# Kernel optimization log

Hardware: AMD Instinct MI355X
Metric: run time of the kernel (lower is better)

Reference implementation:

```python
import jax, jax.numpy as jnp
import numpy as np

B, T, N_EMBED, HEADSIZE = 16, 2048, 1024, 128


def setup_inputs() -> dict:
    key = jax.random.key(0)
    kx, kq, kk, kv = jax.random.split(key, 4)
    x = jax.random.normal(kx, (B, T, N_EMBED), dtype=jnp.float32)
    # nn.Linear(n_embed, headsize, bias=False): y = x @ W, W stored [n_embed, headsize]
    s = (1.0 / np.sqrt(N_EMBED)).astype(np.float32)
    Wq = jax.random.normal(kq, (N_EMBED, HEADSIZE), dtype=jnp.float32) * s
    Wk = jax.random.normal(kk, (N_EMBED, HEADSIZE), dtype=jnp.float32) * s
    Wv = jax.random.normal(kv, (N_EMBED, HEADSIZE), dtype=jnp.float32) * s
    return {"x": x, "Wq": Wq, "Wk": Wk, "Wv": Wv}


def reference(x, Wq, Wk, Wv):
    Bsz, Tlen, C = x.shape
    q = x @ Wq  # [B, T, H]
    k = x @ Wk  # [B, T, H]
    v = x @ Wv  # [B, T, H]
    scale = C ** (-0.5)  # NOTE: original scales by n_embed**-0.5, not headsize**-0.5
    wt = jnp.einsum('bqh,bkh->bqk', q, k) * scale  # [B, T, T]
    causal = jnp.tril(jnp.ones((Tlen, Tlen), dtype=bool))
    wt = jnp.where(causal, wt, -jnp.inf)
    wt = jax.nn.softmax(wt, axis=-1)
    # dropout is identity in eval mode
    out = jnp.einsum('bqk,bkh->bqh', wt, v)  # [B, T, H]
    return out
```

## Files before the change

kernel.cpp:

```cpp
#include <hip/hip_runtime.h>
#include <hip/hip_bf16.h>

#define BATCH 16
#define TLEN 2048
#define CDIM 1024
#define HDIM 128

typedef __attribute__((ext_vector_type(8))) short bf16x8;
typedef __attribute__((ext_vector_type(4))) float f32x4;
typedef __attribute__((ext_vector_type(16))) float f32x16;
typedef __attribute__((ext_vector_type(4))) unsigned short u16x4;
typedef __attribute__((ext_vector_type(8))) unsigned short u16x8;

static __device__ __forceinline__ unsigned short f2bf(float f) {
    __hip_bfloat16 h = __float2bfloat16(f);
    return *(unsigned short*)&h;
}
static __device__ __forceinline__ unsigned pkbf(float a, float b) {
    return (unsigned)f2bf(a) | ((unsigned)f2bf(b) << 16);
}
static __device__ __forceinline__ int part_offs(int qc) {
    const int g = qc >> 2;
    return qc + 2 * g * (g - 1) + (qc & 3) * g;
}

typedef const __attribute__((address_space(1))) unsigned int* gas_t;
typedef __attribute__((address_space(3))) unsigned int* las_t;
static __device__ __forceinline__ void gl_lds16(const void* g, void* l) {
    __builtin_amdgcn_global_load_lds((gas_t)g, (las_t)l, 16, 0, 0);
}

static __device__ __forceinline__ void hard_barrier() {
    __builtin_amdgcn_sched_barrier(0);
    __builtin_amdgcn_s_barrier();
    __builtin_amdgcn_sched_barrier(0);
}

__global__ __launch_bounds__(256) void pack_w(
    const float* __restrict__ Wq, const float* __restrict__ Wk,
    const float* __restrict__ Wv, unsigned short* __restrict__ wtb)
{
    const int which = blockIdx.y;
    const float* W = (which == 0) ? Wq : (which == 1) ? Wk : Wv;
    const int n = blockIdx.x >> 2;
    const int k = (blockIdx.x & 3) * 256 + threadIdx.x;
    wtb[((size_t)which * 128 + n) * 1024 + k] = f2bf(W[(size_t)k * 128 + n]);
}

__global__ __launch_bounds__(512, 4) void qkv_fused(
    const float* __restrict__ x, const unsigned short* __restrict__ wtb,
    unsigned short* __restrict__ qb, unsigned short* __restrict__ kb,
    unsigned short* __restrict__ vtb)
{
    __shared__ __align__(16) unsigned short Ab[2][128 * 64];
    __shared__ __align__(16) unsigned short Bb[2][192 * 64];

    const int xcd = blockIdx.x & 7, s = blockIdx.x >> 3;
    const int m0 = (xcd * 32 + (s >> 1)) * 128;
    const int nh = s & 1;

    const int tid  = threadIdx.x;
    const int lane = tid & 63, wid = tid >> 6;
    const int wm = wid >> 2, wn = wid & 3;
    const int c = lane & 15, g = lane >> 4;

    const int arow = tid >> 2, aq = tid & 3;
    const float* xsrc = x + (size_t)(m0 + arow) * CDIM + aq * 16;

    f32x4 acc[4][3];
#pragma unroll
    for (int i = 0; i < 4; ++i)
#pragma unroll
        for (int j = 0; j < 3; ++j) acc[i][j] = (f32x4){0.f, 0.f, 0.f, 0.f};

    float4 As0, As1, As2, As3;

#define AISSUE(k0_)                                                          \
    { const float* s_ = xsrc + (k0_);                                        \
      As0 = *(const float4*)(s_);      As1 = *(const float4*)(s_ + 4);       \
      As2 = *(const float4*)(s_ + 8);  As3 = *(const float4*)(s_ + 12); }

#define AWRITE(bi_)                                                          \
    { u16x8 t0_, t1_;                                                        \
      t0_[0]=f2bf(As0.x); t0_[1]=f2bf(As0.y); t0_[2]=f2bf(As0.z); t0_[3]=f2bf(As0.w); \
      t0_[4]=f2bf(As1.x); t0_[5]=f2bf(As1.y); t0_[6]=f2bf(As1.z); t0_[7]=f2bf(As1.w); \
      t1_[0]=f2bf(As2.x); t1_[1]=f2bf(As2.y); t1_[2]=f2bf(As2.z); t1_[3]=f2bf(As2.w); \
      t1_[4]=f2bf(As3.x); t1_[5]=f2bf(As3.y); t1_[6]=f2bf(As3.z); t1_[7]=f2bf(As3.w); \
      char* ba_ = (char*)Ab[bi_] + arow * 128;                               \
      *(u16x8*)(ba_ + ((aq * 32 +  0) ^ ((arow & 7) << 4))) = t0_;           \
      *(u16x8*)(ba_ + ((aq * 32 + 16) ^ ((arow & 7) << 4))) = t1_; }

#define BISSUE(k0_, bi_)                                                     \
    { _Pragma("unroll")                                                      \
      for (int i_ = 0; i_ < 3; ++i_) {                                       \
          const int seg_ = wid * 3 + i_;                                     \
          const int row_ = seg_ * 8 + (lane >> 3);                           \
          const int gr_  = (lane & 7) ^ (row_ & 7);                          \
          gl_lds16(wtb + (size_t)(nh * 192 + row_) * 1024 + (k0_) + gr_ * 8, \
                   (char*)Bb[bi_] + seg_ * 1024);                            \
      } }

    AISSUE(0);
    BISSUE(0, 0);
    asm volatile("s_waitcnt vmcnt(3)" ::: "memory");
    AWRITE(0);
    asm volatile("s_waitcnt vmcnt(0) lgkmcnt(0)" ::: "memory");
    hard_barrier();

#pragma unroll 1
    for (int kt = 0; kt < 16; ++kt) {
        const int cur = kt & 1;
        if (kt < 15) {
            AISSUE((kt + 1) * 64);
            BISSUE((kt + 1) * 64, cur ^ 1);
        }

#pragma unroll
        for (int ks = 0; ks < 2; ++ks) {
            bf16x8 af[4], bf[3];
#pragma unroll
            for (int mf = 0; mf < 4; ++mf) {
                const int rm = wm * 64 + mf * 16 + c;
                af[mf] = *(const bf16x8*)((char*)Ab[cur] + rm * 128 +
                                          ((ks * 64 + g * 16) ^ ((rm & 7) << 4)));
            }
#pragma unroll
            for (int nf = 0; nf < 3; ++nf) {
                const int rn = wn * 48 + nf * 16 + c;
                bf[nf] = *(const bf16x8*)((char*)Bb[cur] + rn * 128 +
                                          ((ks * 64 + g * 16) ^ ((rn & 7) << 4)));
            }
            __builtin_amdgcn_s_setprio(1);
#pragma unroll
            for (int mf = 0; mf < 4; ++mf)
#pragma unroll
                for (int nf = 0; nf < 3; ++nf)
                    acc[mf][nf] = __builtin_amdgcn_mfma_f32_16x16x32_bf16(
                        af[mf], bf[nf], acc[mf][nf], 0, 0, 0);
            __builtin_amdgcn_s_setprio(0);
        }

        if (kt < 15) {
            asm volatile("s_waitcnt vmcnt(3)" ::: "memory");
            AWRITE(cur ^ 1);
            asm volatile("s_waitcnt vmcnt(0) lgkmcnt(0)" ::: "memory");
            hard_barrier();
        }
    }

#pragma unroll
    for (int mf = 0; mf < 4; ++mf) {
#pragma unroll
        for (int nf = 0; nf < 3; ++nf) {
            const int col0 = nh * 192 + wn * 48 + nf * 16;
            const int nt = col0 >> 7;
            const int nc = (col0 & 127) + c;
            const int m = m0 + wm * 64 + mf * 16 + g * 4;
            if (nt == 0) {
#pragma unroll
                for (int r = 0; r < 4; ++r)
                    qb[(size_t)(m + r) * HDIM + nc] = f2bf(acc[mf][nf][r] * 0.03125f);
            } else if (nt == 1) {
#pragma unroll
                for (int r = 0; r < 4; ++r)
                    kb[(size_t)(m + r) * HDIM + nc] = f2bf(acc[mf][nf][r]);
            } else {
                const int b = m >> 11, tl = m & (TLEN - 1);
                u16x4 o;
                o[0] = f2bf(acc[mf][nf][0]); o[1] = f2bf(acc[mf][nf][1]);
                o[2] = f2bf(acc[mf][nf][2]); o[3] = f2bf(acc[mf][nf][3]);
                *(u16x4*)(vtb + ((size_t)b * HDIM + nc) * TLEN + tl) = o;
            }
        }
    }
#undef AISSUE
#undef AWRITE
#undef BISSUE
}

__global__ __launch_bounds__(256, 2) void attn_partial(
    const short* __restrict__ qb, const short* __restrict__ kb,
    const short* __restrict__ vtb,
    unsigned short* __restrict__ Opart, float* __restrict__ mpart,
    float* __restrict__ lpart)
{
    const int kc = blockIdx.x;
    const int qc = blockIdx.y;
    const int b  = blockIdx.z;
    if (kc > (qc >> 2)) return;
    const int kv_base = kc * 512;
    const int qrel = qc * 128 - kv_base;
    int NT = (qrel >> 6) + 2; if (NT > 8) NT = 8;

    __shared__ unsigned short Ks[2][64 * 128];
    __shared__ unsigned short Vs[2][128 * 64];

    const int tid  = threadIdx.x;
    const int wid  = tid >> 6;
    const int lane = tid & 63;
    const int c5 = lane & 31, hi = lane >> 5;
    const int q0w = qc * 128 + wid * 32;
    const int qg  = q0w + c5;
    const int pidx = b * 40 + part_offs(qc) + kc;

    const short* Kb  = kb  + (size_t)b * TLEN * HDIM;
    const short* Vtb = vtb + (size_t)b * HDIM * TLEN;

    bf16x8 qf[8];
#pragma unroll
    for (int ks = 0; ks < 8; ++ks)
        qf[ks] = *(const bf16x8*)(qb + ((size_t)b * TLEN + qg) * HDIM + ks * 16 + hi * 8);

    bf16x8 kst[4], vst[4];

#define GLOAD(kv0_)                                                          \
    {                                                                        \
        _Pragma("unroll")                                                    \
        for (int it = 0; it < 4; ++it) {                                     \
            const int o = tid * 16 + it * 4096;                              \
            const int kr = o >> 8, kcb = o & 0xF0;                           \
            kst[it] = *(const bf16x8*)((const char*)Kb +                     \
                        (size_t)((kv0_) + kr) * 256 + kcb);                  \
            const int vr = o >> 7, vcb = o & 0x70;                           \
            vst[it] = *(const bf16x8*)((const char*)Vtb +                    \
                        (size_t)vr * (TLEN * 2) + (size_t)(kv0_) * 2 + vcb); \
        }                                                                    \
    }
#define SSTORE(bi_)                                                          \
    {                                                                        \
        _Pragma("unroll")                                                    \
        for (int it = 0; it < 4; ++it) {                                     \
            const int o = tid * 16 + it * 4096;                              \
            const int kr = o >> 8, kcb = o & 0xF0;                           \
            *(bf16x8*)((char*)Ks[bi_] + kr * 256 + (kcb ^ ((kr & 7) << 4))) = kst[it]; \
            const int vr = o >> 7, vcb = o & 0x70;                           \
            *(bf16x8*)((char*)Vs[bi_] + vr * 128 + (vcb ^ ((vr & 7) << 4))) = vst[it]; \
        }                                                                    \
    }

    GLOAD(kv_base);
    SSTORE(0);
    __syncthreads();

    f32x16 oacc[4];
#pragma unroll
    for (int i = 0; i < 4; ++i)
#pragma unroll
        for (int r = 0; r < 16; ++r) oacc[i][r] = 0.f;
    float m_r = -1e30f;
    float l_r = 0.f;

#pragma unroll 1
    for (int t = 0; t < NT; ++t) {
        const int bi = t & 1;
        if (t + 1 < NT) GLOAD(kv_base + 64 * (t + 1));

        const int kv0 = kv_base + 64 * t;
        if (kv0 <= q0w + 31) {
            f32x16 s0, s1;
#pragma unroll
            for (int r = 0; r < 16; ++r) { s0[r] = 0.f; s1[r] = 0.f; }
            __builtin_amdgcn_s_setprio(1);
#pragma unroll
            for (int ks = 0; ks < 8; ++ks) {
                const int col = ks * 32 + hi * 16;
                const int off0 = c5 * 256 + (col ^ ((c5 & 7) << 4));
                const int off1 = (32 + c5) * 256 + (col ^ ((c5 & 7) << 4));
                bf16x8 a0 = *(const bf16x8*)((char*)Ks[bi] + off0);
                bf16x8 a1 = *(const bf16x8*)((char*)Ks[bi] + off1);
                s0 = __builtin_amdgcn_mfma_f32_32x32x16_bf16(a0, qf[ks], s0, 0, 0, 0);
                s1 = __builtin_amdgcn_mfma_f32_32x32x16_bf16(a1, qf[ks], s1, 0, 0, 0);
            }
            __builtin_amdgcn_s_setprio(0);

            if (kv0 + 63 > q0w) {
#pragma unroll
                for (int r = 0; r < 16; ++r) {
                    const int key0 = kv0 + (r & 3) + 8 * (r >> 2) + 4 * hi;
                    if (key0 > qg)      s0[r] = -INFINITY;
                    if (key0 + 32 > qg) s1[r] = -INFINITY;
                }
            }

            float t8[8];
#pragma unroll
            for (int i = 0; i < 8; ++i)
                t8[i] = fmaxf(fmaxf(s0[2*i], s0[2*i+1]), fmaxf(s1[2*i], s1[2*i+1]));
            float smax = fmaxf(fmaxf(fmaxf(t8[0], t8[1]), fmaxf(t8[2], t8[3])),
                               fmaxf(fmaxf(t8[4], t8[5]), fmaxf(t8[6], t8[7])));
            smax = fmaxf(smax, __shfl_xor(smax, 32));

            const bool defer = __all(smax - m_r <= 8.0f);
            const float mnew = defer ? m_r : fmaxf(m_r, smax);
            if (!defer) {
                const float alpha = __expf(m_r - mnew);
                l_r *= alpha;
#pragma unroll
                for (int hb = 0; hb < 4; ++hb) oacc[hb] = oacc[hb] * alpha;
            }
            m_r = mnew;

#pragma unroll
            for (int r = 0; r < 16; ++r) {
                s0[r] = __expf(s0[r] - mnew);
                s1[r] = __expf(s1[r] - mnew);
            }
            float a8[8];
#pragma unroll
            for (int i = 0; i < 8; ++i)
                a8[i] = (s0[2*i] + s0[2*i+1]) + (s1[2*i] + s1[2*i+1]);
            float psum = ((a8[0] + a8[1]) + (a8[2] + a8[3])) +
                         ((a8[4] + a8[5]) + (a8[6] + a8[7]));
            psum += __shfl_xor(psum, 32);
            l_r += psum;

            bf16x8 pa[4];
#pragma unroll
            for (int kb2 = 0; kb2 < 2; ++kb2) {
#pragma unroll
                for (int par = 0; par < 2; ++par) {
                    const int e = par * 8;
                    float v0, v1, v2, v3, v4, v5, v6, v7;
                    if (kb2 == 0) {
                        v0=s0[e+0]; v1=s0[e+1]; v2=s0[e+2]; v3=s0[e+3];
                        v4=s0[e+4]; v5=s0[e+5]; v6=s0[e+6]; v7=s0[e+7];
                    } else {
                        v0=s1[e+0]; v1=s1[e+1]; v2=s1[e+2]; v3=s1[e+3];
                        v4=s1[e+4]; v5=s1[e+5]; v6=s1[e+6]; v7=s1[e+7];
                    }
                    const unsigned w0 = pkbf(v0, v1), w1 = pkbf(v2, v3);
                    const unsigned w2 = pkbf(v4, v5), w3 = pkbf(v6, v7);
                    const unsigned X0 = hi ? w0 : w2;
                    const unsigned X1 = hi ? w1 : w3;
                    const unsigned R0 = (unsigned)__shfl_xor((int)X0, 32);
                    const unsigned R1 = (unsigned)__shfl_xor((int)X1, 32);
                    union { unsigned w[4]; bf16x8 v; } uu;
                    uu.w[0] = hi ? R0 : w0;  uu.w[1] = hi ? R1 : w1;
                    uu.w[2] = hi ? w2 : R0;  uu.w[3] = hi ? w3 : R1;
                    pa[kb2 * 2 + par] = uu.v;
                }
            }

            __builtin_amdgcn_s_setprio(1);
#pragma unroll
            for (int hb = 0; hb < 4; ++hb) {
                const int row = hb * 32 + c5;
#pragma unroll
                for (int ks = 0; ks < 4; ++ks) {
                    const int off = row * 128 + ((ks * 32 + hi * 16) ^ ((row & 7) << 4));
                    bf16x8 va = *(const bf16x8*)((char*)Vs[bi] + off);
                    oacc[hb] = __builtin_amdgcn_mfma_f32_32x32x16_bf16(va, pa[ks], oacc[hb], 0, 0, 0);
                }
            }
            __builtin_amdgcn_s_setprio(0);
        }

        if (t + 1 < NT) {
            SSTORE(bi ^ 1);
            __syncthreads();
        }
    }

    __syncthreads();
    char* sl = (char*)Ks + wid * 8192;
#pragma unroll
    for (int hb = 0; hb < 4; ++hb)
#pragma unroll
        for (int rq = 0; rq < 4; ++rq) {
            u16x4 o4;
            o4[0] = f2bf(oacc[hb][rq * 4 + 0]);
            o4[1] = f2bf(oacc[hb][rq * 4 + 1]);
            o4[2] = f2bf(oacc[hb][rq * 4 + 2]);
            o4[3] = f2bf(oacc[hb][rq * 4 + 3]);
            const int off = c5 * 256 + ((hb * 64 + rq * 16 + hi * 8) ^ ((c5 & 7) << 4));
            *(u16x4*)(sl + off) = o4;
        }
    asm volatile("s_waitcnt lgkmcnt(0)" ::: "memory");
    __builtin_amdgcn_sched_barrier(0);

    const int qr = lane >> 1, hf = lane & 1;
    unsigned short* Og = Opart + (size_t)pidx * 128 * 128 +
                         (size_t)(wid * 32 + qr) * 128 + hf * 64;
#pragma unroll
    for (int i = 0; i < 8; ++i) {
        const int off = qr * 256 + ((hf * 128 + i * 16) ^ ((qr & 7) << 4));
        *(u16x8*)(Og + i * 8) = *(const u16x8*)(sl + off);
    }
    if (hi == 0) {
        mpart[(size_t)pidx * 128 + wid * 32 + c5] = m_r;
        lpart[(size_t)pidx * 128 + wid * 32 + c5] = l_r;
    }
#undef GLOAD
#undef SSTORE
}

__global__ __launch_bounds__(256) void attn_combine(
    const unsigned short* __restrict__ Opart, const float* __restrict__ mpart,
    const float* __restrict__ lpart, float* __restrict__ out)
{
    const int qc = blockIdx.x;
    const int b  = blockIdx.y;
    const int n  = (qc >> 2) + 1;
    const int base = b * 40 + part_offs(qc);
    const int t   = threadIdx.x;
    const int row = t >> 1;
    const int d0  = (t & 1) * 64;

    float mv[4], lv[4];
#pragma unroll
    for (int p = 0; p < 4; ++p) {
        mv[p] = (p < n) ? mpart[(size_t)(base + p) * 128 + row] : -INFINITY;
        lv[p] = (p < n) ? lpart[(size_t)(base + p) * 128 + row] : 0.f;
    }
    float M = fmaxf(fmaxf(mv[0], mv[1]), fmaxf(mv[2], mv[3]));
    float L = 0.f;
    float wv[4];
#pragma unroll
    for (int p = 0; p < 4; ++p) {
        wv[p] = (p < n) ? __expf(mv[p] - M) : 0.f;
        L += wv[p] * lv[p];
    }

    float acc[64];
#pragma unroll
    for (int i = 0; i < 64; ++i) acc[i] = 0.f;

    for (int p = 0; p < n; ++p) {
        const float w = wv[p];
        const bf16x8* src = (const bf16x8*)(Opart +
            ((size_t)(base + p) * 128 + row) * 128 + d0);
#pragma unroll
        for (int j = 0; j < 8; ++j) {
            bf16x8 v = src[j];
#pragma unroll
            for (int e = 0; e < 8; ++e) {
                union { unsigned u; float f; } xx;
                xx.u = ((unsigned)(unsigned short)v[e]) << 16;
                acc[j * 8 + e] += w * xx.f;
            }
        }
    }

    const float invL = 1.f / L;
    float4* dst = (float4*)(out + ((size_t)(b * TLEN + qc * 128 + row)) * 128 + d0);
#pragma unroll
    for (int i = 0; i < 16; ++i)
        dst[i] = make_float4(acc[4*i] * invL, acc[4*i+1] * invL,
                             acc[4*i+2] * invL, acc[4*i+3] * invL);
}

extern "C" void kernel_launch(void* const* d_in, const int* in_sizes, int n_in,
                              void* d_out, int out_size, void* d_ws, size_t ws_size,
                              hipStream_t stream)
{
    const float* x  = (const float*)d_in[0];
    const float* Wq = (const float*)d_in[1];
    const float* Wk = (const float*)d_in[2];
    const float* Wv = (const float*)d_in[3];
    float* outp = (float*)d_out;

    const size_t per = (size_t)BATCH * TLEN * HDIM;
    unsigned short* qb  = (unsigned short*)d_ws;
    unsigned short* kb  = qb + per;
    unsigned short* vtb = kb + per;
    unsigned short* wtb = vtb + per;
    unsigned short* Opart = wtb + 384 * 1024;
    float* mpart = (float*)(Opart + (size_t)640 * 128 * 128);
    float* lpart = mpart + (size_t)640 * 128;

    dim3 gw(512, 3);
    pack_w<<<gw, 256, 0, stream>>>(Wq, Wk, Wv, wtb);

    qkv_fused<<<512, 512, 0, stream>>>(x, wtb, qb, kb, vtb);

    dim3 g2(4, 16, BATCH);
    attn_partial<<<g2, 256, 0, stream>>>((const short*)qb, (const short*)kb,
                                         (const short*)vtb, Opart, mpart, lpart);

    dim3 g3(16, BATCH);
    attn_combine<<<g3, 256, 0, stream>>>(Opart, mpart, lpart, outp);
}
```

Baseline: 112.8 us.

## Double QKV projection M-tile to 256 rows to improve weight reuse

```diff
diff --git a/kernel.cpp b/kernel.cpp
--- a/kernel.cpp
+++ b/kernel.cpp
@@ -47,16 +47,16 @@
     wtb[((size_t)which * 128 + n) * 1024 + k] = f2bf(W[(size_t)k * 128 + n]);
 }
 
-__global__ __launch_bounds__(512, 4) void qkv_fused(
+__global__ __launch_bounds__(512, 2) void qkv_fused(
     const float* __restrict__ x, const unsigned short* __restrict__ wtb,
     unsigned short* __restrict__ qb, unsigned short* __restrict__ kb,
     unsigned short* __restrict__ vtb)
 {
-    __shared__ __align__(16) unsigned short Ab[2][128 * 64];
+    __shared__ __align__(16) unsigned short Ab[2][256 * 64];
     __shared__ __align__(16) unsigned short Bb[2][192 * 64];
 
     const int xcd = blockIdx.x & 7, s = blockIdx.x >> 3;
-    const int m0 = (xcd * 32 + (s >> 1)) * 128;
+    const int m0 = (xcd * 16 + (s >> 1)) * 256;
     const int nh = s & 1;
 
     const int tid  = threadIdx.x;
@@ -64,31 +64,37 @@
     const int wm = wid >> 2, wn = wid & 3;
     const int c = lane & 15, g = lane >> 4;
 
-    const int arow = tid >> 2, aq = tid & 3;
-    const float* xsrc = x + (size_t)(m0 + arow) * CDIM + aq * 16;
-
-    f32x4 acc[4][3];
-#pragma unroll
-    for (int i = 0; i < 4; ++i)
+    const int arow = tid >> 1, ah = tid & 1;
+    const float* xsrc = x + (size_t)(m0 + arow) * CDIM + ah * 32;
+
+    f32x4 acc[8][3];
+#pragma unroll
+    for (int i = 0; i < 8; ++i)
 #pragma unroll
         for (int j = 0; j < 3; ++j) acc[i][j] = (f32x4){0.f, 0.f, 0.f, 0.f};
 
-    float4 As0, As1, As2, As3;
+    float4 As0, As1, As2, As3, As4, As5, As6, As7;
 
 #define AISSUE(k0_)                                                          \
     { const float* s_ = xsrc + (k0_);                                        \
-      As0 = *(const float4*)(s_);      As1 = *(const float4*)(s_ + 4);       \
-      As2 = *(const float4*)(s_ + 8);  As3 = *(const float4*)(s_ + 12); }
+      As0 = *(const float4*)(s_);       As1 = *(const float4*)(s_ + 4);      \
+      As2 = *(const float4*)(s_ + 8);   As3 = *(const float4*)(s_ + 12);     \
+      As4 = *(const float4*)(s_ + 16);  As5 = *(const float4*)(s_ + 20);     \
+      As6 = *(const float4*)(s_ + 24);  As7 = *(const float4*)(s_ + 28); }
+
+#define CVT2(lo_, hi_, dst_)                                                 \
+    { u16x8 t_;                                                              \
+      t_[0]=f2bf(lo_.x); t_[1]=f2bf(lo_.y); t_[2]=f2bf(lo_.z); t_[3]=f2bf(lo_.w); \
+      t_[4]=f2bf(hi_.x); t_[5]=f2bf(hi_.y); t_[6]=f2bf(hi_.z); t_[7]=f2bf(hi_.w); \
+      *(u16x8*)(dst_) = t_; }
 
 #define AWRITE(bi_)                                                          \
-    { u16x8 t0_, t1_;                                                        \
-      t0_[0]=f2bf(As0.x); t0_[1]=f2bf(As0.y); t0_[2]=f2bf(As0.z); t0_[3]=f2bf(As0.w); \
-      t0_[4]=f2bf(As1.x); t0_[5]=f2bf(As1.y); t0_[6]=f2bf(As1.z); t0_[7]=f2bf(As1.w); \
-      t1_[0]=f2bf(As2.x); t1_[1]=f2bf(As2.y); t1_[2]=f2bf(As2.z); t1_[3]=f2bf(As2.w); \
-      t1_[4]=f2bf(As3.x); t1_[5]=f2bf(As3.y); t1_[6]=f2bf(As3.z); t1_[7]=f2bf(As3.w); \
-      char* ba_ = (char*)Ab[bi_] + arow * 128;                               \
-      *(u16x8*)(ba_ + ((aq * 32 +  0) ^ ((arow & 7) << 4))) = t0_;           \
-      *(u16x8*)(ba_ + ((aq * 32 + 16) ^ ((arow & 7) << 4))) = t1_; }
+    { char* ba_ = (char*)Ab[bi_] + arow * 128;                               \
+      const int sw_ = (arow & 7) << 4;                                       \
+      CVT2(As0, As1, ba_ + ((ah * 64 +  0) ^ sw_));                          \
+      CVT2(As2, As3, ba_ + ((ah * 64 + 16) ^ sw_));                          \
+      CVT2(As4, As5, ba_ + ((ah * 64 + 32) ^ sw_));                          \
+      CVT2(As6, As7, ba_ + ((ah * 64 + 48) ^ sw_)); }
 
 #define BISSUE(k0_, bi_)                                                     \
     { _Pragma("unroll")                                                      \
@@ -117,10 +123,10 @@
 
 #pragma unroll
         for (int ks = 0; ks < 2; ++ks) {
-            bf16x8 af[4], bf[3];
-#pragma unroll
-            for (int mf = 0; mf < 4; ++mf) {
-                const int rm = wm * 64 + mf * 16 + c;
+            bf16x8 af[8], bf[3];
+#pragma unroll
+            for (int mf = 0; mf < 8; ++mf) {
+                const int rm = wm * 128 + mf * 16 + c;
                 af[mf] = *(const bf16x8*)((char*)Ab[cur] + rm * 128 +
                                           ((ks * 64 + g * 16) ^ ((rm & 7) << 4)));
             }
@@ -132,7 +138,7 @@
             }
             __builtin_amdgcn_s_setprio(1);
 #pragma unroll
-            for (int mf = 0; mf < 4; ++mf)
+            for (int mf = 0; mf < 8; ++mf)
 #pragma unroll
                 for (int nf = 0; nf < 3; ++nf)
                     acc[mf][nf] = __builtin_amdgcn_mfma_f32_16x16x32_bf16(
@@ -149,13 +155,13 @@
     }
 
 #pragma unroll
-    for (int mf = 0; mf < 4; ++mf) {
+    for (int mf = 0; mf < 8; ++mf) {
 #pragma unroll
         for (int nf = 0; nf < 3; ++nf) {
             const int col0 = nh * 192 + wn * 48 + nf * 16;
             const int nt = col0 >> 7;
             const int nc = (col0 & 127) + c;
-            const int m = m0 + wm * 64 + mf * 16 + g * 4;
+            const int m = m0 + wm * 128 + mf * 16 + g * 4;
             if (nt == 0) {
 #pragma unroll
                 for (int r = 0; r < 4; ++r)
@@ -174,6 +180,7 @@
         }
     }
 #undef AISSUE
+#undef CVT2
 #undef AWRITE
 #undef BISSUE
 }
@@ -471,7 +478,7 @@
     dim3 gw(512, 3);
     pack_w<<<gw, 256, 0, stream>>>(Wq, Wk, Wv, wtb);
 
-    qkv_fused<<<512, 512, 0, stream>>>(x, wtb, qb, kb, vtb);
+    qkv_fused<<<256, 512, 0, stream>>>(x, wtb, qb, kb, vtb);
 
     dim3 g2(4, 16, BATCH);
     attn_partial<<<g2, 256, 0, stream>>>((const short*)qb, (const short*)kb,
```

After: 136.8 us. +21.2%, slower.

## Share K/V tiles across two query chunks per 512-thread attention block

Applied to the files above, without the earlier changes.

```diff
diff --git a/kernel.cpp b/kernel.cpp
--- a/kernel.cpp
+++ b/kernel.cpp
@@ -178,30 +178,32 @@
 #undef BISSUE
 }
 
-__global__ __launch_bounds__(256, 2) void attn_partial(
+__global__ __launch_bounds__(512, 2) void attn_partial(
     const short* __restrict__ qb, const short* __restrict__ kb,
     const short* __restrict__ vtb,
     unsigned short* __restrict__ Opart, float* __restrict__ mpart,
     float* __restrict__ lpart)
 {
-    const int kc = blockIdx.x;
-    const int qc = blockIdx.y;
-    const int b  = blockIdx.z;
-    if (kc > (qc >> 2)) return;
+    const int kc  = blockIdx.x;
+    const int qc2 = blockIdx.y;
+    const int b   = blockIdx.z;
+    if (kc > (qc2 >> 1)) return;
     const int kv_base = kc * 512;
-    const int qrel = qc * 128 - kv_base;
-    int NT = (qrel >> 6) + 2; if (NT > 8) NT = 8;
-
-    __shared__ unsigned short Ks[2][64 * 128];
-    __shared__ unsigned short Vs[2][128 * 64];
+    int NT = ((qc2 * 256 - kv_base) >> 6) + 4; if (NT > 8) NT = 8;
+
+    __shared__ unsigned short KV[2][16384];
+#define KSB(bi_) ((char*)KV[bi_])
+#define VSB(bi_) ((char*)KV[bi_] + 16384)
 
     const int tid  = threadIdx.x;
     const int wid  = tid >> 6;
     const int lane = tid & 63;
     const int c5 = lane & 31, hi = lane >> 5;
-    const int q0w = qc * 128 + wid * 32;
+    const int half = wid >> 2, wq = wid & 3;
+    const int qc_eff = qc2 * 2 + half;
+    const int q0w = qc2 * 256 + wid * 32;
     const int qg  = q0w + c5;
-    const int pidx = b * 40 + part_offs(qc) + kc;
+    const int pidx = b * 40 + part_offs(qc_eff) + kc;
 
     const short* Kb  = kb  + (size_t)b * TLEN * HDIM;
     const short* Vtb = vtb + (size_t)b * HDIM * TLEN;
@@ -211,13 +213,13 @@
     for (int ks = 0; ks < 8; ++ks)
         qf[ks] = *(const bf16x8*)(qb + ((size_t)b * TLEN + qg) * HDIM + ks * 16 + hi * 8);
 
-    bf16x8 kst[4], vst[4];
+    bf16x8 kst[2], vst[2];
 
 #define GLOAD(kv0_)                                                          \
     {                                                                        \
         _Pragma("unroll")                                                    \
-        for (int it = 0; it < 4; ++it) {                                     \
-            const int o = tid * 16 + it * 4096;                              \
+        for (int it = 0; it < 2; ++it) {                                     \
+            const int o = tid * 16 + it * 8192;                              \
             const int kr = o >> 8, kcb = o & 0xF0;                           \
             kst[it] = *(const bf16x8*)((const char*)Kb +                     \
                         (size_t)((kv0_) + kr) * 256 + kcb);                  \
@@ -229,12 +231,12 @@
 #define SSTORE(bi_)                                                          \
     {                                                                        \
         _Pragma("unroll")                                                    \
-        for (int it = 0; it < 4; ++it) {                                     \
-            const int o = tid * 16 + it * 4096;                              \
+        for (int it = 0; it < 2; ++it) {                                     \
+            const int o = tid * 16 + it * 8192;                              \
             const int kr = o >> 8, kcb = o & 0xF0;                           \
-            *(bf16x8*)((char*)Ks[bi_] + kr * 256 + (kcb ^ ((kr & 7) << 4))) = kst[it]; \
+            *(bf16x8*)(KSB(bi_) + kr * 256 + (kcb ^ ((kr & 7) << 4))) = kst[it]; \
             const int vr = o >> 7, vcb = o & 0x70;                           \
-            *(bf16x8*)((char*)Vs[bi_] + vr * 128 + (vcb ^ ((vr & 7) << 4))) = vst[it]; \
+            *(bf16x8*)(VSB(bi_) + vr * 128 + (vcb ^ ((vr & 7) << 4))) = vst[it]; \
         }                                                                    \
     }
 
@@ -266,8 +268,8 @@
                 const int col = ks * 32 + hi * 16;
                 const int off0 = c5 * 256 + (col ^ ((c5 & 7) << 4));
                 const int off1 = (32 + c5) * 256 + (col ^ ((c5 & 7) << 4));
-                bf16x8 a0 = *(const bf16x8*)((char*)Ks[bi] + off0);
-                bf16x8 a1 = *(const bf16x8*)((char*)Ks[bi] + off1);
+                bf16x8 a0 = *(const bf16x8*)(KSB(bi) + off0);
+                bf16x8 a1 = *(const bf16x8*)(KSB(bi) + off1);
                 s0 = __builtin_amdgcn_mfma_f32_32x32x16_bf16(a0, qf[ks], s0, 0, 0, 0);
                 s1 = __builtin_amdgcn_mfma_f32_32x32x16_bf16(a1, qf[ks], s1, 0, 0, 0);
             }
@@ -348,7 +350,7 @@
 #pragma unroll
                 for (int ks = 0; ks < 4; ++ks) {
                     const int off = row * 128 + ((ks * 32 + hi * 16) ^ ((row & 7) << 4));
-                    bf16x8 va = *(const bf16x8*)((char*)Vs[bi] + off);
+                    bf16x8 va = *(const bf16x8*)(VSB(bi) + off);
                     oacc[hb] = __builtin_amdgcn_mfma_f32_32x32x16_bf16(va, pa[ks], oacc[hb], 0, 0, 0);
                 }
             }
@@ -362,7 +364,7 @@
     }
 
     __syncthreads();
-    char* sl = (char*)Ks + wid * 8192;
+    char* sl = (char*)KV + wid * 8192;
 #pragma unroll
     for (int hb = 0; hb < 4; ++hb)
 #pragma unroll
@@ -380,18 +382,20 @@
 
     const int qr = lane >> 1, hf = lane & 1;
     unsigned short* Og = Opart + (size_t)pidx * 128 * 128 +
-                         (size_t)(wid * 32 + qr) * 128 + hf * 64;
+                         (size_t)(wq * 32 + qr) * 128 + hf * 64;
 #pragma unroll
     for (int i = 0; i < 8; ++i) {
         const int off = qr * 256 + ((hf * 128 + i * 16) ^ ((qr & 7) << 4));
         *(u16x8*)(Og + i * 8) = *(const u16x8*)(sl + off);
     }
     if (hi == 0) {
-        mpart[(size_t)pidx * 128 + wid * 32 + c5] = m_r;
-        lpart[(size_t)pidx * 128 + wid * 32 + c5] = l_r;
+        mpart[(size_t)pidx * 128 + wq * 32 + c5] = m_r;
+        lpart[(size_t)pidx * 128 + wq * 32 + c5] = l_r;
     }
 #undef GLOAD
 #undef SSTORE
+#undef KSB
+#undef VSB
 }
 
 __global__ __launch_bounds__(256) void attn_combine(
@@ -473,8 +477,8 @@
 
     qkv_fused<<<512, 512, 0, stream>>>(x, wtb, qb, kb, vtb);
 
-    dim3 g2(4, 16, BATCH);
-    attn_partial<<<g2, 256, 0, stream>>>((const short*)qb, (const short*)kb,
+    dim3 g2(4, 8, BATCH);
+    attn_partial<<<g2, 512, 0, stream>>>((const short*)qb, (const short*)kb,
                                          (const short*)vtb, Opart, mpart, lpart);
 
     dim3 g3(16, BATCH);
```

Result: slower. 115.3 us (+2.2%).
